# Kernel optimization log

Measured on AMD Instinct MI355X. Metric: run time of the kernel, lower is better.

## Reference

```python
import jax, jax.numpy as jnp
import numpy as np

N_NODES = 40000
N_EDGES = 640000
IN_CH = 128
HID = 128
OUT_CH = 16
N_GRAPHS = 64
EPS = 1e-16


def segment_softmax(logits, seg, num_segments):
    m = jax.ops.segment_max(logits, seg, num_segments=num_segments)
    e = jnp.exp(logits - m[seg])
    s = jax.ops.segment_sum(e, seg, num_segments=num_segments)
    return e / (s[seg] + EPS)


def gt_conv(x, src, dst, W, b, att):
    # x: [N, Cin] -> h: [N, C]
    h = x @ W + b
    s = h @ att  # [N] per-node attention score (att broadcast over rows)
    # alpha_e = <x_i, att> + <x_j, att>; x_i = target (dst), x_j = source (src)
    alpha = s[dst] + s[src]
    alpha = jax.nn.leaky_relu(alpha, negative_slope=0.2)
    # PyG code normalizes over edge_index[0] groups (source nodes)
    alpha = segment_softmax(alpha, src, x.shape[0])
    msg = h[src] * alpha[:, None]
    return jax.ops.segment_sum(msg, dst, num_segments=x.shape[0])


def gcn_conv(x, src, dst, W, b):
    n = x.shape[0]
    h = x @ W
    deg = jax.ops.segment_sum(jnp.ones_like(src, dtype=h.dtype), dst, num_segments=n)
    dinv = jnp.where(deg > 0, deg ** -0.5, 0.0)
    norm = dinv[src] * dinv[dst]
    out = jax.ops.segment_sum(h[src] * norm[:, None], dst, num_segments=n)
    return out + b


def setup_inputs() -> dict:
    key = jax.random.key(0)
    ks = jax.random.split(key, 12)
    x = jax.random.normal(ks[0], (N_NODES, IN_CH), dtype=jnp.float32)
    edge_index = jax.random.randint(ks[1], (2, N_EDGES), 0, N_NODES, dtype=jnp.int32)
    batch = jnp.sort(jax.random.randint(ks[2], (N_NODES,), 0, N_GRAPHS, dtype=jnp.int32))
    def glorot(k, shape):
        fan_in, fan_out = shape[0], shape[-1]
        lim = jnp.sqrt(6.0 / (fan_in + fan_out))
        return jax.random.uniform(k, shape, jnp.float32, -lim, lim)
    return {
        "x": x, "edge_index": edge_index, "batch": batch,
        "W1": glorot(ks[3], (IN_CH, HID)), "b1": jnp.zeros((HID,), jnp.float32),
        "att1": glorot(ks[4], (1, HID))[0],
        "W2": glorot(ks[5], (HID, HID)), "b2": jnp.zeros((HID,), jnp.float32),
        "att2": glorot(ks[6], (1, HID))[0],
        "Wg": glorot(ks[7], (HID, HID)), "bg": jnp.zeros((HID,), jnp.float32),
        "Wfc": glorot(ks[8], (HID, OUT_CH)), "bfc": jnp.zeros((OUT_CH,), jnp.float32),
    }


def reference(x, edge_index, batch, W1, b1, att1, W2, b2, att2, Wg, bg, Wfc, bfc):
    n = x.shape[0]
    loops = jnp.arange(n, dtype=edge_index.dtype)
    src = jnp.concatenate([edge_index[0], loops])
    dst = jnp.concatenate([edge_index[1], loops])
    # two GT layers (dropout is identity in eval mode)
    h = jax.nn.relu(gt_conv(x, src, dst, W1, b1, att1))
    h = jax.nn.relu(gt_conv(h, src, dst, W2, b2, att2))
    # GCNConv (with self loops, symmetric normalization)
    h = gcn_conv(h, src, dst, Wg, bg)
    # global mean pool over graphs
    sums = jax.ops.segment_sum(h, batch, num_segments=N_GRAPHS)
    counts = jax.ops.segment_sum(jnp.ones((n,), h.dtype), batch, num_segments=N_GRAPHS)
    pooled = sums / jnp.maximum(counts, 1.0)[:, None]
    logits = pooled @ Wfc + bfc
    return jax.nn.log_softmax(logits, axis=1)
```

## Files before the change

### kernel.cpp

```cpp
#include <hip/hip_runtime.h>
#include <hip/hip_fp16.h>
#include <hip/hip_fp8.h>
#include <math.h>

#define NN 40000
#define NE 640000
#define ET 680000
#define CH 128
#define OC 16
#define NG 64
#define NQ (ET/4)
#define CAP 48
#define NBKT 8
#define BKT_DIV 5000
#define NFILLB 5320
#define NGEMMB 625
#define NGRP 79
#define GRP 72
#define NBLK1 (NGRP*GRP + (NFILLB - NGRP*64))

typedef _Float16 h8 __attribute__((ext_vector_type(8)));
typedef float    f4 __attribute__((ext_vector_type(4)));

__device__ __forceinline__ float2 fp8x2_to_f32(unsigned short v) {
    __hip_fp8_e4m3 a, b;
    a.__x = (__hip_fp8_storage_t)(v & 0xff);
    b.__x = (__hip_fp8_storage_t)(v >> 8);
    return make_float2((float)a, (float)b);
}
__device__ __forceinline__ unsigned char f32_to_fp8(float f) {
    __hip_fp8_e4m3 t(f);
    return (unsigned char)t.__x;
}

__global__ __launch_bounds__(256)
void prep(const int* __restrict__ batch, int* __restrict__ gstart,
          int* __restrict__ cur_d, int* __restrict__ cur_s,
          float* __restrict__ pooled,
          const float* __restrict__ W1, const float* __restrict__ W2,
          const float* __restrict__ Wg, _Float16* __restrict__ Wt1,
          _Float16* __restrict__ Wt2, _Float16* __restrict__ Wtg)
{
    int i = blockIdx.x * 256 + threadIdx.x;
    if (i < NN) {
        cur_d[i] = 0; cur_s[i] = 0;
        int b = batch[i];
        if (i == 0) { for (int g = 0; g <= b; ++g) gstart[g] = 0; }
        else { int pb = batch[i - 1]; for (int g = pb + 1; g <= b; ++g) gstart[g] = i; }
        if (i == NN - 1) { for (int g = b + 1; g <= NG; ++g) gstart[g] = NN; }
    }
    if (i < NG * CH) pooled[i] = 0.f;
    if (i < CH * CH) {
        int k = i >> 7, n = i & 127;
        Wt1[n * CH + k] = (_Float16)W1[i];
        Wt2[n * CH + k] = (_Float16)W2[i];
        Wtg[n * CH + k] = (_Float16)Wg[i];
    }
}

__device__ __forceinline__
void stage_w(_Float16 (*wt)[136], const _Float16* __restrict__ Wt, int tid)
{
#pragma unroll
    for (int i = 0; i < 8; ++i) {
        int f = tid + i * 256;
        int n = f >> 4, c8 = f & 15;
        *(float4*)&wt[n][c8 * 8] = *(const float4*)(Wt + (size_t)n * CH + c8 * 8);
    }
}

template<bool BIAS, bool ATTN>
__device__ __forceinline__
void mfma_body(_Float16 (*xs)[136], _Float16 (*wt)[136],
               const float* __restrict__ bias, const float* __restrict__ att,
               unsigned char* __restrict__ out8, float* __restrict__ s,
               int rb, int tid)
{
    const int wv = tid >> 6, lane = tid & 63;
    const int m = lane & 15, quad = lane >> 4;
    f4 acc[8] = {};
#pragma unroll
    for (int ks = 0; ks < 4; ++ks) {
        h8 a = *(const h8*)&xs[wv * 16 + m][ks * 32 + quad * 8];
#pragma unroll
        for (int t = 0; t < 8; ++t) {
            h8 b = *(const h8*)&wt[t * 16 + m][ks * 32 + quad * 8];
            acc[t] = __builtin_amdgcn_mfma_f32_16x16x32_f16(a, b, acc[t], 0, 0, 0);
        }
    }
    float pr[4] = {0.f, 0.f, 0.f, 0.f};
#pragma unroll
    for (int t = 0; t < 8; ++t) {
        int col = t * 16 + m;
        float bv = BIAS ? bias[col] : 0.f;
        float av = ATTN ? att[col] : 0.f;
#pragma unroll
        for (int r = 0; r < 4; ++r) {
            float o = acc[t][r] + bv;
            int row = rb + wv * 16 + quad * 4 + r;
            out8[(size_t)row * CH + col] = f32_to_fp8(o);
            if (ATTN) pr[r] += o * av;
        }
    }
    if (ATTN) {
#pragma unroll
        for (int r = 0; r < 4; ++r) {
            float p = pr[r];
            p += __shfl_xor(p, 1); p += __shfl_xor(p, 2);
            p += __shfl_xor(p, 4); p += __shfl_xor(p, 8);
            if (m == 0) s[rb + wv * 16 + quad * 4 + r] = p;
        }
    }
}

__device__ __forceinline__
void fill_body(int fb, int tid, const int* __restrict__ ei,
               int* __restrict__ cur_d, int* __restrict__ cur_s,
               unsigned short* __restrict__ pad_src,
               unsigned short* __restrict__ pad_dst)
{
    int bkt = fb & (NBKT - 1);
    int q = (fb >> 3) * 256 + tid;
    if (q >= NQ) return;
    int e0 = q * 4;
    int4 sv, dv;
    if (e0 < NE) {
        sv = *(const int4*)(ei + e0);
        dv = *(const int4*)(ei + NE + e0);
    } else {
        int b = e0 - NE;
        sv = make_int4(b, b + 1, b + 2, b + 3);
        dv = sv;
    }
    const int* sc = (const int*)&sv;
    const int* dc = (const int*)&dv;
#pragma unroll
    for (int u = 0; u < 4; ++u) {
        int srcE = sc[u], dstE = dc[u];
        if ((unsigned)dstE / BKT_DIV == (unsigned)bkt) {
            int p = atomicAdd(cur_d + dstE, 1);
            if (p < CAP) pad_src[dstE * CAP + p] = (unsigned short)srcE;
        }
        if ((unsigned)srcE / BKT_DIV == (unsigned)bkt) {
            int p = atomicAdd(cur_s + srcE, 1);
            if (p < CAP) pad_dst[srcE * CAP + p] = (unsigned short)dstE;
        }
    }
}

__global__ __launch_bounds__(256)
void fill_gemm1(const float* __restrict__ x, const _Float16* __restrict__ Wt1,
                const float* __restrict__ b1, const float* __restrict__ att1,
                unsigned char* __restrict__ out8, float* __restrict__ s1,
                const int* __restrict__ ei, int* __restrict__ cur_d,
                int* __restrict__ cur_s, unsigned short* __restrict__ pad_src,
                unsigned short* __restrict__ pad_dst)
{
    __shared__ __attribute__((aligned(16))) _Float16 xs[64][136];
    __shared__ __attribute__((aligned(16))) _Float16 wt[128][136];
    int grp = blockIdx.x / GRP, o = blockIdx.x % GRP;
    if (grp < NGRP && o < 8) {
        int g = grp * 8 + o;
        if (g < NGEMMB) {
            int rb = g * 64, tid = threadIdx.x;
#pragma unroll
            for (int i = 0; i < 4; ++i) {
                int f = tid + i * 256;
                int r = f >> 4, c8 = f & 15;
                const float* p = x + (size_t)(rb + r) * CH + c8 * 8;
                float4 v0 = *(const float4*)p;
                float4 v1 = *(const float4*)(p + 4);
                __half2 h[4] = { __floats2half2_rn(v0.x, v0.y), __floats2half2_rn(v0.z, v0.w),
                                 __floats2half2_rn(v1.x, v1.y), __floats2half2_rn(v1.z, v1.w) };
                *(float4*)&xs[r][c8 * 8] = *(float4*)h;
            }
            stage_w(wt, Wt1, tid);
            __syncthreads();
            mfma_body<true, true>(xs, wt, b1, att1, out8, s1, rb, tid);
        }
        return;
    }
    int fb = (grp < NGRP) ? grp * 64 + (o - 8)
                          : NGRP * 64 + (blockIdx.x - NGRP * GRP);
    if (fb < NFILLB)
        fill_body(fb, threadIdx.x, ei, cur_d, cur_s, pad_src, pad_dst);
}

template<bool RELU, bool BIAS, bool ATTN>
__global__ __launch_bounds__(256)
void gemm_k(const __half* __restrict__ in, const _Float16* __restrict__ Wt,
            const float* __restrict__ bias, const float* __restrict__ att,
            unsigned char* __restrict__ out8, float* __restrict__ s)
{
    __shared__ __attribute__((aligned(16))) _Float16 xs[64][136];
    __shared__ __attribute__((aligned(16))) _Float16 wt[128][136];
    const int tid = threadIdx.x;
    const int rb = blockIdx.x * 64;
#pragma unroll
    for (int i = 0; i < 4; ++i) {
        int f = tid + i * 256;
        int r = f >> 4, c8 = f & 15;
        float4 raw = *(const float4*)(in + (size_t)(rb + r) * CH + c8 * 8);
        if (RELU) {
            __half2* h2 = (__half2*)&raw;
#pragma unroll
            for (int u = 0; u < 4; ++u) {
                float2 fv = __half22float2(h2[u]);
                h2[u] = __floats2half2_rn(fmaxf(fv.x, 0.f), fmaxf(fv.y, 0.f));
            }
        }
        *(float4*)&xs[r][c8 * 8] = raw;
    }
    stage_w(wt, Wt, tid);
    __syncthreads();
    mfma_body<BIAS, ATTN>(xs, wt, bias, att, out8, s, rb, tid);
}

__global__ __launch_bounds__(256)
void softmax_stats(const int* __restrict__ cur_s,
                   const unsigned short* __restrict__ pad_dst,
                   const float* __restrict__ s, float* __restrict__ ssum)
{
    int node = (blockIdx.x * 256 + threadIdx.x) >> 6;
    int lane = threadIdx.x & 63;
    if (node >= NN) return;
    int deg = min(cur_s[node], CAP);
    float si = s[node];
    float sum = 0.f;
    if (lane < deg) {
        int d = pad_dst[node * CAP + lane];
        float t = si + s[d];
        t = t > 0.f ? t : 0.2f * t;
        sum = expf(t);
    }
#pragma unroll
    for (int o = 32; o; o >>= 1) sum += __shfl_xor(sum, o);
    if (lane == 0) ssum[node] = sum;
}

__device__ __forceinline__
void gather_core(int node, int lane, int deg, int src, float w,
                 const unsigned char* __restrict__ h8p, __half* __restrict__ out16)
{
    int qtr = lane >> 4, cl = lane & 15;
    float a[8] = {};
    for (int base = 0; base < deg; base += 8) {
        uint2 v[2]; float wj[2];
#pragma unroll
        for (int u = 0; u < 2; ++u) {
            int e = base + 4 * u + qtr;
            int sj = __shfl(src, e);
            wj[u]  = __shfl(w, e);
            v[u] = ((const uint2*)(h8p + (size_t)sj * CH))[cl];
        }
#pragma unroll
        for (int u = 0; u < 2; ++u) {
            float2 p0 = fp8x2_to_f32((unsigned short)(v[u].x & 0xffff));
            float2 p1 = fp8x2_to_f32((unsigned short)(v[u].x >> 16));
            float2 p2 = fp8x2_to_f32((unsigned short)(v[u].y & 0xffff));
            float2 p3 = fp8x2_to_f32((unsigned short)(v[u].y >> 16));
            a[0] += p0.x * wj[u]; a[1] += p0.y * wj[u];
            a[2] += p1.x * wj[u]; a[3] += p1.y * wj[u];
            a[4] += p2.x * wj[u]; a[5] += p2.y * wj[u];
            a[6] += p3.x * wj[u]; a[7] += p3.y * wj[u];
        }
    }
#pragma unroll
    for (int k = 0; k < 8; ++k) {
        a[k] += __shfl_xor(a[k], 16);
        a[k] += __shfl_xor(a[k], 32);
    }
    if (qtr == 0) {
        float4 st;
        ((__half2*)&st)[0] = __floats2half2_rn(a[0], a[1]);
        ((__half2*)&st)[1] = __floats2half2_rn(a[2], a[3]);
        ((__half2*)&st)[2] = __floats2half2_rn(a[4], a[5]);
        ((__half2*)&st)[3] = __floats2half2_rn(a[6], a[7]);
        ((float4*)(out16 + (size_t)node * CH))[cl] = st;
    }
}

__global__ __launch_bounds__(256)
void gt_gather(const int* __restrict__ cur_d,
               const unsigned short* __restrict__ pad_src,
               const unsigned char* __restrict__ h8p, const float* __restrict__ s,
               const float* __restrict__ ssum, __half* __restrict__ out16)
{
    int node = (blockIdx.x * 256 + threadIdx.x) >> 6;
    int lane = threadIdx.x & 63;
    if (node >= NN) return;
    int deg = min(cur_d[node], CAP);
    float sd = s[node];
    int src = 0; float w = 0.f;
    if (lane < deg) {
        src = pad_src[node * CAP + lane];
        float t = sd + s[src];
        t = t > 0.f ? t : 0.2f * t;
        w = expf(t) / ssum[src];
    }
    gather_core(node, lane, deg, src, w, h8p, out16);
}

__global__ __launch_bounds__(256)
void gcn_gather(const int* __restrict__ cur_d,
                const unsigned short* __restrict__ pad_src,
                const unsigned char* __restrict__ h8p, __half* __restrict__ out16)
{
    int node = (blockIdx.x * 256 + threadIdx.x) >> 6;
    int lane = threadIdx.x & 63;
    if (node >= NN) return;
    int dn = cur_d[node];
    int deg = min(dn, CAP);
    float nu = rsqrtf((float)max(dn, 1));
    int src = 0; float w = 0.f;
    if (lane < deg) {
        src = pad_src[node * CAP + lane];
        w = rsqrtf((float)max(cur_d[src], 1)) * nu;
    }
    gather_core(node, lane, deg, src, w, h8p, out16);
}

__global__ __launch_bounds__(128)
void pool_part(const __half* __restrict__ h16, const int* __restrict__ batch,
               float* __restrict__ pooled)
{
    int ch = threadIdx.x;
    int start = blockIdx.x * 80;
    float acc = 0.f;
    int curg = batch[start];
    for (int base = start; base < start + 80; base += 8) {
        float vals[8]; int gs[8];
#pragma unroll
        for (int u = 0; u < 8; ++u)
            vals[u] = __half2float(h16[(size_t)(base + u) * CH + ch]);
#pragma unroll
        for (int u = 0; u < 8; ++u) gs[u] = batch[base + u];
#pragma unroll
        for (int u = 0; u < 8; ++u) {
            if (gs[u] != curg) {
                atomicAdd(pooled + (size_t)curg * CH + ch, acc);
                acc = 0.f; curg = gs[u];
            }
            acc += vals[u];
        }
    }
    atomicAdd(pooled + (size_t)curg * CH + ch, acc);
}

__global__ __launch_bounds__(256)
void head_kernel(const float* __restrict__ psum, const int* __restrict__ gstart,
                 const float* __restrict__ bg, const float* __restrict__ Wfc,
                 const float* __restrict__ bfc, float* __restrict__ out)
{
    __shared__ float lg[NG][OC];
    int tid = threadIdx.x;
#pragma unroll
    for (int i = 0; i < 4; ++i) {
        int f = tid + i * 256;
        int g = f >> 4, o = f & 15;
        float cnt = fmaxf((float)(gstart[g + 1] - gstart[g]), 1.0f);
        float inv = 1.0f / cnt;
        float acc = bfc[o];
        for (int c = 0; c < CH; ++c)
            acc += (psum[g * CH + c] * inv + bg[c]) * Wfc[c * OC + o];
        lg[g][o] = acc;
    }
    __syncthreads();
    if (tid < NG) {
        float m = -1e30f;
#pragma unroll
        for (int o = 0; o < OC; ++o) m = fmaxf(m, lg[tid][o]);
        float sum = 0.f;
#pragma unroll
        for (int o = 0; o < OC; ++o) sum += expf(lg[tid][o] - m);
        float lse = m + logf(sum);
#pragma unroll
        for (int o = 0; o < OC; ++o) out[tid * OC + o] = lg[tid][o] - lse;
    }
}

extern "C" void kernel_launch(void* const* d_in, const int* in_sizes, int n_in,
                              void* d_out, int out_size, void* d_ws, size_t ws_size,
                              hipStream_t stream)
{
    const float* x     = (const float*)d_in[0];
    const int*   ei    = (const int*)d_in[1];
    const int*   batch = (const int*)d_in[2];
    const float* W1    = (const float*)d_in[3];
    const float* b1    = (const float*)d_in[4];
    const float* att1  = (const float*)d_in[5];
    const float* W2    = (const float*)d_in[6];
    const float* b2    = (const float*)d_in[7];
    const float* att2  = (const float*)d_in[8];
    const float* Wg    = (const float*)d_in[9];
    const float* bg    = (const float*)d_in[10];
    const float* Wfc   = (const float*)d_in[11];
    const float* bfc   = (const float*)d_in[12];
    float* out = (float*)d_out;

    const size_t NNCH = (size_t)NN * CH;
    __half* B16 = (__half*)d_ws;
    unsigned char* A8 = (unsigned char*)(B16 + NNCH);
    _Float16* Wt1 = (_Float16*)(A8 + NNCH);
    _Float16* Wt2 = Wt1 + CH * CH;
    _Float16* Wtg = Wt2 + CH * CH;
    int*   cur_d  = (int*)(Wtg + CH * CH);
    int*   cur_s  = cur_d + NN;
    float* s1     = (float*)(cur_s + NN);
    float* s2     = s1 + NN;
    float* pooled = s2 + NN;
    float* ssum   = pooled + NG * CH;
    int*   gstart = (int*)(ssum + NN);
    unsigned short* pad_src = (unsigned short*)(gstart + NG + 1);
    unsigned short* pad_dst = pad_src + (size_t)NN * CAP;

    const int WB = NN / 4;

    prep<<<157, 256, 0, stream>>>(batch, gstart, cur_d, cur_s, pooled,
                                  W1, W2, Wg, Wt1, Wt2, Wtg);

    fill_gemm1<<<NBLK1, 256, 0, stream>>>(
        x, Wt1, b1, att1, A8, s1, ei, cur_d, cur_s, pad_src, pad_dst);
    softmax_stats<<<WB, 256, 0, stream>>>(cur_s, pad_dst, s1, ssum);
    gt_gather<<<WB, 256, 0, stream>>>(cur_d, pad_src, A8, s1, ssum, B16);

    gemm_k<true, true, true><<<NGEMMB, 256, 0, stream>>>(
        B16, Wt2, b2, att2, A8, s2);
    softmax_stats<<<WB, 256, 0, stream>>>(cur_s, pad_dst, s2, ssum);
    gt_gather<<<WB, 256, 0, stream>>>(cur_d, pad_src, A8, s2, ssum, B16);

    gemm_k<true, false, false><<<NGEMMB, 256, 0, stream>>>(
        B16, Wtg, nullptr, nullptr, A8, nullptr);
    gcn_gather<<<WB, 256, 0, stream>>>(cur_d, pad_src, A8, B16);

    pool_part<<<500, 128, 0, stream>>>(B16, batch, pooled);
    head_kernel<<<1, 256, 0, stream>>>(pooled, gstart, bg, Wfc, bfc, out);
}
```

Measured before the change: 271.0 us.

## Drop LDS staging in fused fill+GEMM1 kernel, load MFMA operands directly

The first-layer GEMM inside the fused fill/GEMM kernel now feeds MFMA operands straight from global memory (x as nontemporal loads, W from global/L2) instead of staging both through 52KB of shared memory with a barrier. Removing the LDS arrays lets the fill blocks, which share the kernel, run at much higher occupancy, and a launch-bounds hint of 6 blocks per CU is added. The edge-index loads in the fill path also become nontemporal. The trade-off is redundant global/L2 reads of W per wave and less coalesced x loads in the GEMM path.

```diff
diff --git a/kernel.cpp b/kernel.cpp
--- a/kernel.cpp
+++ b/kernel.cpp
@@ -21,6 +21,7 @@
 
 typedef _Float16 h8 __attribute__((ext_vector_type(8)));
 typedef float    f4 __attribute__((ext_vector_type(4)));
+typedef int      i4 __attribute__((ext_vector_type(4)));
 
 __device__ __forceinline__ float2 fp8x2_to_f32(unsigned short v) {
     __hip_fp8_e4m3 a, b;
@@ -113,6 +114,59 @@
     }
 }
 
+template<bool BIAS, bool ATTN>
+__device__ __forceinline__
+void gemm_direct(const float* __restrict__ x, const _Float16* __restrict__ Wt,
+                 const float* __restrict__ bias, const float* __restrict__ att,
+                 unsigned char* __restrict__ out8, float* __restrict__ s,
+                 int rb, int tid)
+{
+    const int wv = tid >> 6, lane = tid & 63;
+    const int m = lane & 15, quad = lane >> 4;
+    const int arow = rb + wv * 16 + m;
+    const float* xp = x + (size_t)arow * CH + quad * 8;
+    const _Float16* wbase = Wt + m * CH + quad * 8;
+    f4 acc[8] = {};
+#pragma unroll
+    for (int ks = 0; ks < 4; ++ks) {
+        f4 v0 = __builtin_nontemporal_load((const f4*)(xp + ks * 32));
+        f4 v1 = __builtin_nontemporal_load((const f4*)(xp + ks * 32) + 1);
+        h8 a;
+        a[0] = (_Float16)v0[0]; a[1] = (_Float16)v0[1];
+        a[2] = (_Float16)v0[2]; a[3] = (_Float16)v0[3];
+        a[4] = (_Float16)v1[0]; a[5] = (_Float16)v1[1];
+        a[6] = (_Float16)v1[2]; a[7] = (_Float16)v1[3];
+#pragma unroll
+        for (int t = 0; t < 8; ++t) {
+            h8 b = *(const h8*)(wbase + t * 16 * CH + ks * 32);
+            acc[t] = __builtin_amdgcn_mfma_f32_16x16x32_f16(a, b, acc[t], 0, 0, 0);
+        }
+    }
+    float pr[4] = {0.f, 0.f, 0.f, 0.f};
+#pragma unroll
+    for (int t = 0; t < 8; ++t) {
+        int col = t * 16 + m;
+        float bv = BIAS ? bias[col] : 0.f;
+        float av = ATTN ? att[col] : 0.f;
+#pragma unroll
+        for (int r = 0; r < 4; ++r) {
+            float o = acc[t][r] + bv;
+            int row = rb + wv * 16 + quad * 4 + r;
+            out8[(size_t)row * CH + col] = f32_to_fp8(o);
+            if (ATTN) pr[r] += o * av;
+        }
+    }
+    if (ATTN) {
+#pragma unroll
+        for (int r = 0; r < 4; ++r) {
+            float p = pr[r];
+            p += __shfl_xor(p, 1); p += __shfl_xor(p, 2);
+            p += __shfl_xor(p, 4); p += __shfl_xor(p, 8);
+            if (m == 0) s[rb + wv * 16 + quad * 4 + r] = p;
+        }
+    }
+}
+
 __device__ __forceinline__
 void fill_body(int fb, int tid, const int* __restrict__ ei,
                int* __restrict__ cur_d, int* __restrict__ cur_s,
@@ -123,20 +177,18 @@
     int q = (fb >> 3) * 256 + tid;
     if (q >= NQ) return;
     int e0 = q * 4;
-    int4 sv, dv;
+    i4 sv, dv;
     if (e0 < NE) {
-        sv = *(const int4*)(ei + e0);
-        dv = *(const int4*)(ei + NE + e0);
+        sv = __builtin_nontemporal_load((const i4*)(ei + e0));
+        dv = __builtin_nontemporal_load((const i4*)(ei + NE + e0));
     } else {
         int b = e0 - NE;
-        sv = make_int4(b, b + 1, b + 2, b + 3);
+        sv = (i4){b, b + 1, b + 2, b + 3};
         dv = sv;
     }
-    const int* sc = (const int*)&sv;
-    const int* dc = (const int*)&dv;
 #pragma unroll
     for (int u = 0; u < 4; ++u) {
-        int srcE = sc[u], dstE = dc[u];
+        int srcE = sv[u], dstE = dv[u];
         if ((unsigned)dstE / BKT_DIV == (unsigned)bkt) {
             int p = atomicAdd(cur_d + dstE, 1);
             if (p < CAP) pad_src[dstE * CAP + p] = (unsigned short)srcE;
@@ -148,7 +200,7 @@
     }
 }
 
-__global__ __launch_bounds__(256)
+__global__ __launch_bounds__(256, 6)
 void fill_gemm1(const float* __restrict__ x, const _Float16* __restrict__ Wt1,
                 const float* __restrict__ b1, const float* __restrict__ att1,
                 unsigned char* __restrict__ out8, float* __restrict__ s1,
@@ -156,28 +208,12 @@
                 int* __restrict__ cur_s, unsigned short* __restrict__ pad_src,
                 unsigned short* __restrict__ pad_dst)
 {
-    __shared__ __attribute__((aligned(16))) _Float16 xs[64][136];
-    __shared__ __attribute__((aligned(16))) _Float16 wt[128][136];
     int grp = blockIdx.x / GRP, o = blockIdx.x % GRP;
     if (grp < NGRP && o < 8) {
         int g = grp * 8 + o;
-        if (g < NGEMMB) {
-            int rb = g * 64, tid = threadIdx.x;
-#pragma unroll
-            for (int i = 0; i < 4; ++i) {
-                int f = tid + i * 256;
-                int r = f >> 4, c8 = f & 15;
-                const float* p = x + (size_t)(rb + r) * CH + c8 * 8;
-                float4 v0 = *(const float4*)p;
-                float4 v1 = *(const float4*)(p + 4);
-                __half2 h[4] = { __floats2half2_rn(v0.x, v0.y), __floats2half2_rn(v0.z, v0.w),
-                                 __floats2half2_rn(v1.x, v1.y), __floats2half2_rn(v1.z, v1.w) };
-                *(float4*)&xs[r][c8 * 8] = *(float4*)h;
-            }
-            stage_w(wt, Wt1, tid);
-            __syncthreads();
-            mfma_body<true, true>(xs, wt, b1, att1, out8, s1, rb, tid);
-        }
+        if (g < NGEMMB)
+            gemm_direct<true, true>(x, Wt1, b1, att1, out8, s1, g * 64,
+                                    threadIdx.x);
         return;
     }
     int fb = (grp < NGRP) ? grp * 64 + (o - 8)
```

New measurement: 283.2 us. 1.04x slower.

## Replace source-side CSR and softmax stats with edge-parallel atomic exp sums

Applied to the files above, without the earlier changes.

Drops the per-source padded adjacency (pad_dst, cur_s) built during the fill phase. The softmax denominators are now computed by an edge-parallel kernel that reads edge_index directly and atomically adds exp(leaky_relu) into ssum, which the GEMM epilogue zeroes first. This removes half of the fill atomics and scattered writes plus the wave-per-node stats kernel. In exchange it adds 680k float atomics per layer and makes the summation order nondeterministic. It also removes the CAP truncation on source degree, so it no longer matches the previous padded behaviour exactly.

```diff
diff --git a/kernel.cpp b/kernel.cpp
--- a/kernel.cpp
+++ b/kernel.cpp
@@ -18,6 +18,7 @@
 #define NGRP 79
 #define GRP 72
 #define NBLK1 (NGRP*GRP + (NFILLB - NGRP*64))
+#define NQB 665
 
 typedef _Float16 h8 __attribute__((ext_vector_type(8)));
 typedef float    f4 __attribute__((ext_vector_type(4)));
@@ -35,15 +36,14 @@
 
 __global__ __launch_bounds__(256)
 void prep(const int* __restrict__ batch, int* __restrict__ gstart,
-          int* __restrict__ cur_d, int* __restrict__ cur_s,
-          float* __restrict__ pooled,
+          int* __restrict__ cur_d, float* __restrict__ pooled,
           const float* __restrict__ W1, const float* __restrict__ W2,
           const float* __restrict__ Wg, _Float16* __restrict__ Wt1,
           _Float16* __restrict__ Wt2, _Float16* __restrict__ Wtg)
 {
     int i = blockIdx.x * 256 + threadIdx.x;
     if (i < NN) {
-        cur_d[i] = 0; cur_s[i] = 0;
+        cur_d[i] = 0;
         int b = batch[i];
         if (i == 0) { for (int g = 0; g <= b; ++g) gstart[g] = 0; }
         else { int pb = batch[i - 1]; for (int g = pb + 1; g <= b; ++g) gstart[g] = i; }
@@ -74,7 +74,7 @@
 void mfma_body(_Float16 (*xs)[136], _Float16 (*wt)[136],
                const float* __restrict__ bias, const float* __restrict__ att,
                unsigned char* __restrict__ out8, float* __restrict__ s,
-               int rb, int tid)
+               float* __restrict__ ss0, int rb, int tid)
 {
     const int wv = tid >> 6, lane = tid & 63;
     const int m = lane & 15, quad = lane >> 4;
@@ -108,16 +108,18 @@
             float p = pr[r];
             p += __shfl_xor(p, 1); p += __shfl_xor(p, 2);
             p += __shfl_xor(p, 4); p += __shfl_xor(p, 8);
-            if (m == 0) s[rb + wv * 16 + quad * 4 + r] = p;
+            if (m == 0) {
+                int row = rb + wv * 16 + quad * 4 + r;
+                s[row] = p;
+                ss0[row] = 0.f;
+            }
         }
     }
 }
 
 __device__ __forceinline__
 void fill_body(int fb, int tid, const int* __restrict__ ei,
-               int* __restrict__ cur_d, int* __restrict__ cur_s,
-               unsigned short* __restrict__ pad_src,
-               unsigned short* __restrict__ pad_dst)
+               int* __restrict__ cur_d, unsigned short* __restrict__ pad_src)
 {
     int bkt = fb & (NBKT - 1);
     int q = (fb >> 3) * 256 + tid;
@@ -141,10 +143,6 @@
             int p = atomicAdd(cur_d + dstE, 1);
             if (p < CAP) pad_src[dstE * CAP + p] = (unsigned short)srcE;
         }
-        if ((unsigned)srcE / BKT_DIV == (unsigned)bkt) {
-            int p = atomicAdd(cur_s + srcE, 1);
-            if (p < CAP) pad_dst[srcE * CAP + p] = (unsigned short)dstE;
-        }
     }
 }
 
@@ -152,9 +150,8 @@
 void fill_gemm1(const float* __restrict__ x, const _Float16* __restrict__ Wt1,
                 const float* __restrict__ b1, const float* __restrict__ att1,
                 unsigned char* __restrict__ out8, float* __restrict__ s1,
-                const int* __restrict__ ei, int* __restrict__ cur_d,
-                int* __restrict__ cur_s, unsigned short* __restrict__ pad_src,
-                unsigned short* __restrict__ pad_dst)
+                float* __restrict__ ssum, const int* __restrict__ ei,
+                int* __restrict__ cur_d, unsigned short* __restrict__ pad_src)
 {
     __shared__ __attribute__((aligned(16))) _Float16 xs[64][136];
     __shared__ __attribute__((aligned(16))) _Float16 wt[128][136];
@@ -176,21 +173,22 @@
             }
             stage_w(wt, Wt1, tid);
             __syncthreads();
-            mfma_body<true, true>(xs, wt, b1, att1, out8, s1, rb, tid);
+            mfma_body<true, true>(xs, wt, b1, att1, out8, s1, ssum, rb, tid);
         }
         return;
     }
     int fb = (grp < NGRP) ? grp * 64 + (o - 8)
                           : NGRP * 64 + (blockIdx.x - NGRP * GRP);
     if (fb < NFILLB)
-        fill_body(fb, threadIdx.x, ei, cur_d, cur_s, pad_src, pad_dst);
+        fill_body(fb, threadIdx.x, ei, cur_d, pad_src);
 }
 
 template<bool RELU, bool BIAS, bool ATTN>
 __global__ __launch_bounds__(256)
 void gemm_k(const __half* __restrict__ in, const _Float16* __restrict__ Wt,
             const float* __restrict__ bias, const float* __restrict__ att,
-            unsigned char* __restrict__ out8, float* __restrict__ s)
+            unsigned char* __restrict__ out8, float* __restrict__ s,
+            float* __restrict__ ss0)
 {
     __shared__ __attribute__((aligned(16))) _Float16 xs[64][136];
     __shared__ __attribute__((aligned(16))) _Float16 wt[128][136];
@@ -213,29 +211,36 @@
     }
     stage_w(wt, Wt, tid);
     __syncthreads();
-    mfma_body<BIAS, ATTN>(xs, wt, bias, att, out8, s, rb, tid);
-}
-
-__global__ __launch_bounds__(256)
-void softmax_stats(const int* __restrict__ cur_s,
-                   const unsigned short* __restrict__ pad_dst,
-                   const float* __restrict__ s, float* __restrict__ ssum)
-{
-    int node = (blockIdx.x * 256 + threadIdx.x) >> 6;
-    int lane = threadIdx.x & 63;
-    if (node >= NN) return;
-    int deg = min(cur_s[node], CAP);
-    float si = s[node];
-    float sum = 0.f;
-    if (lane < deg) {
-        int d = pad_dst[node * CAP + lane];
-        float t = si + s[d];
+    mfma_body<BIAS, ATTN>(xs, wt, bias, att, out8, s, ss0, rb, tid);
+}
+
+__global__ __launch_bounds__(256)
+void edge_ssum(const int* __restrict__ ei, const float* __restrict__ s,
+               float* __restrict__ ssum)
+{
+    int q = blockIdx.x * 256 + threadIdx.x;
+    if (q >= NQ) return;
+    int e0 = q * 4;
+    int4 sv, dv;
+    if (e0 < NE) {
+        sv = *(const int4*)(ei + e0);
+        dv = *(const int4*)(ei + NE + e0);
+    } else {
+        int b = e0 - NE;
+        sv = make_int4(b, b + 1, b + 2, b + 3);
+        dv = sv;
+    }
+    const int* sc = (const int*)&sv;
+    const int* dc = (const int*)&dv;
+    float ssrc[4], sdst[4];
+#pragma unroll
+    for (int u = 0; u < 4; ++u) { ssrc[u] = s[sc[u]]; sdst[u] = s[dc[u]]; }
+#pragma unroll
+    for (int u = 0; u < 4; ++u) {
+        float t = ssrc[u] + sdst[u];
         t = t > 0.f ? t : 0.2f * t;
-        sum = expf(t);
-    }
-#pragma unroll
-    for (int o = 32; o; o >>= 1) sum += __shfl_xor(sum, o);
-    if (lane == 0) ssum[node] = sum;
+        atomicAdd(ssum + sc[u], expf(t));
+    }
 }
 
 __device__ __forceinline__
@@ -405,32 +410,30 @@
     _Float16* Wt2 = Wt1 + CH * CH;
     _Float16* Wtg = Wt2 + CH * CH;
     int*   cur_d  = (int*)(Wtg + CH * CH);
-    int*   cur_s  = cur_d + NN;
-    float* s1     = (float*)(cur_s + NN);
+    float* s1     = (float*)(cur_d + NN);
     float* s2     = s1 + NN;
     float* pooled = s2 + NN;
     float* ssum   = pooled + NG * CH;
     int*   gstart = (int*)(ssum + NN);
     unsigned short* pad_src = (unsigned short*)(gstart + NG + 1);
-    unsigned short* pad_dst = pad_src + (size_t)NN * CAP;
 
     const int WB = NN / 4;
 
-    prep<<<157, 256, 0, stream>>>(batch, gstart, cur_d, cur_s, pooled,
+    prep<<<157, 256, 0, stream>>>(batch, gstart, cur_d, pooled,
                                   W1, W2, Wg, Wt1, Wt2, Wtg);
 
     fill_gemm1<<<NBLK1, 256, 0, stream>>>(
-        x, Wt1, b1, att1, A8, s1, ei, cur_d, cur_s, pad_src, pad_dst);
-    softmax_stats<<<WB, 256, 0, stream>>>(cur_s, pad_dst, s1, ssum);
+        x, Wt1, b1, att1, A8, s1, ssum, ei, cur_d, pad_src);
+    edge_ssum<<<NQB, 256, 0, stream>>>(ei, s1, ssum);
     gt_gather<<<WB, 256, 0, stream>>>(cur_d, pad_src, A8, s1, ssum, B16);
 
     gemm_k<true, true, true><<<NGEMMB, 256, 0, stream>>>(
-        B16, Wt2, b2, att2, A8, s2);
-    softmax_stats<<<WB, 256, 0, stream>>>(cur_s, pad_dst, s2, ssum);
+        B16, Wt2, b2, att2, A8, s2, ssum);
+    edge_ssum<<<NQB, 256, 0, stream>>>(ei, s2, ssum);
     gt_gather<<<WB, 256, 0, stream>>>(cur_d, pad_src, A8, s2, ssum, B16);
 
     gemm_k<true, false, false><<<NGEMMB, 256, 0, stream>>>(
-        B16, Wtg, nullptr, nullptr, A8, nullptr);
+        B16, Wtg, nullptr, nullptr, A8, nullptr, nullptr);
     gcn_gather<<<WB, 256, 0, stream>>>(cur_d, pad_src, A8, B16);
 
     pool_part<<<500, 128, 0, stream>>>(B16, batch, pooled);
```

After: 300.5 us. +10.9%, slower.
